# Kernel tuning notes

Measured on AMD Instinct MI355X. Metric: run time of the kernel, lower is better.

## Reference

```python
import jax, jax.numpy as jnp
import numpy as np

N0 = 1373      # hardcoded node-type split in the original forward
TAO = 0.4
EPS = 1e-12


def _l2norm(x, axis):
    # matches torch F.normalize(p=2): x / max(||x||, eps)
    n = jnp.sqrt(jnp.sum(x * x, axis=axis, keepdims=True))
    return x / jnp.maximum(n, EPS)


def setup_inputs() -> dict:
    key = jax.random.key(0)
    ks = jax.random.split(key, 12)
    N, E, D_IN, F, H, D = 20000, 320000, 256, 32, 8, 32
    feat = jax.random.normal(ks[0], (N, D_IN), jnp.float32)
    sloc = jax.random.normal(ks[1], (N, D), jnp.float32)
    topo_fea = jax.random.normal(ks[2], (N, D), jnp.float32)
    src = jax.random.randint(ks[3], (E,), 0, N)
    dst = jax.random.randint(ks[4], (E,), 0, N)
    e_feat = jax.random.randint(ks[5], (E,), 0, 4)
    s = 1.0 / np.sqrt(D_IN)
    W_proj0 = jax.random.normal(ks[6], (D_IN, H * F), jnp.float32) * s
    W_proj1 = jax.random.normal(ks[7], (D_IN, H * F), jnp.float32) * s
    W_prob = jax.random.normal(ks[8], (H, F, F), jnp.float32) * (1.0 / np.sqrt(F))
    W_res0 = jax.random.normal(ks[9], (D_IN, H * F), jnp.float32) * s
    W_res1 = jax.random.normal(ks[10], (D_IN, H * F), jnp.float32) * s
    etype_attn = jnp.ones((4,), jnp.float32)
    return dict(feat=feat, sloc=sloc, topo_fea=topo_fea, src=src, dst=dst,
                e_feat=e_feat, W_proj0=W_proj0, W_proj1=W_proj1, W_prob=W_prob,
                W_res0=W_res0, W_res1=W_res1, etype_attn=etype_attn)


def reference(feat, sloc, topo_fea, src, dst, e_feat,
              W_proj0, W_proj1, W_prob, W_res0, W_res1, etype_attn):
    N = feat.shape[0]
    H, F = W_prob.shape[0], W_prob.shape[2]
    sloc3 = sloc[:, None, :]        # (N,1,D) -- .unsqueeze(1)
    topo3 = topo_fea[:, None, :]

    # per-type node projection
    feat_src = jnp.concatenate(
        [feat[:N0] @ W_proj0, feat[N0:] @ W_proj1], axis=0).reshape(N, H, F)
    # per-head attention feature: softmax(tanh(fc4prob_i(.)), dim=feat)
    ft_attn = jax.nn.softmax(
        jnp.tanh(jnp.einsum('nhf,hfg->nhg', feat_src, W_prob)), axis=2)
    # F.normalize over the NODE dimension (dim=0), as in original
    ft_norm = _l2norm(feat_src, axis=0)

    sloc_n = _l2norm(sloc3, axis=2)
    topo_n = _l2norm(topo3, axis=2)

    # edge attention scores
    a = jnp.sum(ft_attn[dst] * ft_norm[src], axis=2, keepdims=True)   # (E,H,1)
    cos_s = jnp.sum(sloc_n[src] * sloc_n[dst], axis=2, keepdims=True)  # (E,1,1)
    cos_t = jnp.sum(topo_n[src] * topo_n[dst], axis=2, keepdims=True)
    sim = (TAO * cos_s + (1.0 - TAO) * cos_t + 1.0) / 2.0             # (E,1,1)
    e = (sim * a * etype_attn[e_feat][:, None, None])[:, :, 0]        # (E,H)

    # edge softmax: segment softmax over incoming edges of each dst node
    m = jax.ops.segment_max(e, dst, num_segments=N)                   # (N,H)
    ex = jnp.exp(e - m[dst])
    z = jax.ops.segment_sum(ex, dst, num_segments=N)
    att = ex / z[dst]                                                 # (E,H)

    # three u_mul_e + sum aggregations
    aw = att[:, :, None]                                              # (E,H,1)
    rst = jax.ops.segment_sum(feat_src[src] * aw, dst, num_segments=N)  # (N,H,F)
    sl2 = jax.ops.segment_sum(sloc3[src] * aw, dst, num_segments=N)     # (N,H,D)
    tp2 = jax.ops.segment_sum(topo3[src] * aw, dst, num_segments=N)     # (N,H,D)

    resval = jnp.concatenate(
        [feat[:N0] @ W_res0, feat[N0:] @ W_res1], axis=0).reshape(N, H, F)
    out_fea = jax.nn.relu(rst + resval).mean(axis=1)   # (N,F)
    out_sloc = (sl2 + sloc3).mean(axis=1)              # (N,D)
    out_topo = (tp2 + topo3).mean(axis=1)              # (N,D)
    return out_fea, out_sloc, out_topo
```

## Files before the change

kernel.cpp:

```cpp
#include <hip/hip_runtime.h>
#include <math.h>

#define HN0 1373
#define BM 128
#define BN 128
#define BK 32
#define LDT 40

typedef __attribute__((ext_vector_type(8))) short short8;
typedef __attribute__((ext_vector_type(4))) float f32x4;

__device__ inline unsigned short f2bf(float f) {
  unsigned int u = __float_as_uint(f);
  unsigned int r = (u + 0x7FFFu + ((u >> 16) & 1u)) >> 16;
  return (unsigned short)r;
}
__device__ inline float bflo(unsigned int u) { return __uint_as_float(u << 16); }
__device__ inline float bfhi(unsigned int u) { return __uint_as_float(u & 0xFFFF0000u); }

__device__ inline uint4 pack8bf(float4 a, float4 b) {
  uint4 o;
  o.x = (unsigned)f2bf(a.x) | ((unsigned)f2bf(a.y) << 16);
  o.y = (unsigned)f2bf(a.z) | ((unsigned)f2bf(a.w) << 16);
  o.z = (unsigned)f2bf(b.x) | ((unsigned)f2bf(b.y) << 16);
  o.w = (unsigned)f2bf(b.z) | ((unsigned)f2bf(b.w) << 16);
  return o;
}

__global__ __launch_bounds__(256) void prep(
    const float* __restrict__ Wp0, const float* __restrict__ Wr0,
    const float* __restrict__ Wp1, const float* __restrict__ Wr1,
    unsigned short* __restrict__ BTw,
    const float* __restrict__ sloc, const float* __restrict__ topo,
    float* __restrict__ inv_s, float* __restrict__ inv_t,
    unsigned short* __restrict__ slt,
    const int* __restrict__ dst, int* __restrict__ deg, int N, int E) {
  int b = blockIdx.x;
  int tid = threadIdx.x;
  int nodeBlocks = (N + 7) / 8;
  if (b < 1024) {
    int n = b & 511, g = b >> 9;
    const float* W;
    if (g == 0) W = (n < 256) ? Wp0 : Wr0;
    else        W = (n < 256) ? Wp1 : Wr1;
    int c = n & 255;
    BTw[(size_t)g * 512 * 256 + (size_t)n * 256 + tid] = f2bf(W[(size_t)tid * 256 + c]);
  } else if (b < 1024 + nodeBlocks) {
    int node = (b - 1024) * 8 + (tid >> 5);
    int d = tid & 31;
    if (node >= N) return;
    float s = sloc[(size_t)node * 32 + d];
    float t = topo[(size_t)node * 32 + d];
    float ss = s * s, tt = t * t;
#pragma unroll
    for (int m = 16; m >= 1; m >>= 1) {
      ss += __shfl_xor(ss, m);
      tt += __shfl_xor(tt, m);
    }
    if (d == 0) {
      inv_s[node] = 1.f / fmaxf(sqrtf(ss), 1e-12f);
      inv_t[node] = 1.f / fmaxf(sqrtf(tt), 1e-12f);
    }
    slt[(size_t)node * 64 + d] = f2bf(s);
    slt[(size_t)node * 64 + 32 + d] = f2bf(t);
  } else {
    int e = (b - 1024 - nodeBlocks) * 256 + tid;
    if (e < E) atomicAdd(&deg[dst[e]], 1);
  }
}

__global__ __launch_bounds__(256) void gemm_mfma(
    const float* __restrict__ A, const unsigned short* __restrict__ BTw,
    unsigned short* __restrict__ feat_bf, float* __restrict__ resval, int N) {
  __shared__ __align__(16) unsigned short As[BM * LDT];
  __shared__ __align__(16) unsigned short Bs[BN * LDT];
  int tid = threadIdx.x;
  int lane = tid & 63;
  int w = tid >> 6;
  int wr = w >> 1, wc = w & 1;

  int g0t = (HN0 + BM - 1) / BM;
  int bx = blockIdx.x;
  bool g1 = bx >= g0t;
  int rowBase = g1 ? HN0 + (bx - g0t) * BM : bx * BM;
  int rowEnd = g1 ? N : HN0;
  const unsigned short* BT = BTw + (g1 ? (size_t)512 * 256 : 0);
  int colBase = blockIdx.y * BN;

  int r0 = tid >> 2;
  int kp = (tid & 3) << 3;
  int ar1 = min(rowBase + r0, rowEnd - 1);
  int ar2 = min(rowBase + r0 + 64, rowEnd - 1);
  const float* aP1 = A + (size_t)ar1 * 256 + kp;
  const float* aP2 = A + (size_t)ar2 * 256 + kp;
  const unsigned short* bP1 = BT + (size_t)(colBase + r0) * 256 + kp;
  const unsigned short* bP2 = bP1 + (size_t)64 * 256;
  int wo1 = r0 * LDT + kp;
  int wo2 = (r0 + 64) * LDT + kp;

  int q = lane >> 4;
  int fr = lane & 15;
  int aOff = (wr * 64 + fr) * LDT + q * 8;
  int bOff = (wc * 64 + fr) * LDT + q * 8;

  f32x4 acc[4][4] = {};

  float4 fa1a = *reinterpret_cast<const float4*>(aP1);
  float4 fa1b = *reinterpret_cast<const float4*>(aP1 + 4);
  float4 fa2a = *reinterpret_cast<const float4*>(aP2);
  float4 fa2b = *reinterpret_cast<const float4*>(aP2 + 4);
  uint4 rb1 = *reinterpret_cast<const uint4*>(bP1);
  uint4 rb2 = *reinterpret_cast<const uint4*>(bP2);

  for (int t = 0; t < 8; ++t) {
    *reinterpret_cast<uint4*>(&As[wo1]) = pack8bf(fa1a, fa1b);
    *reinterpret_cast<uint4*>(&As[wo2]) = pack8bf(fa2a, fa2b);
    *reinterpret_cast<uint4*>(&Bs[wo1]) = rb1;
    *reinterpret_cast<uint4*>(&Bs[wo2]) = rb2;
    __syncthreads();
    if (t < 7) {
      int ko = (t + 1) * BK;
      fa1a = *reinterpret_cast<const float4*>(aP1 + ko);
      fa1b = *reinterpret_cast<const float4*>(aP1 + ko + 4);
      fa2a = *reinterpret_cast<const float4*>(aP2 + ko);
      fa2b = *reinterpret_cast<const float4*>(aP2 + ko + 4);
      rb1 = *reinterpret_cast<const uint4*>(bP1 + ko);
      rb2 = *reinterpret_cast<const uint4*>(bP2 + ko);
    }
    short8 af[4], bf4[4];
#pragma unroll
    for (int i = 0; i < 4; ++i) {
      af[i] = *reinterpret_cast<const short8*>(&As[aOff + i * 16 * LDT]);
      bf4[i] = *reinterpret_cast<const short8*>(&Bs[bOff + i * 16 * LDT]);
    }
#pragma unroll
    for (int i = 0; i < 4; ++i)
#pragma unroll
      for (int j = 0; j < 4; ++j)
        acc[i][j] = __builtin_amdgcn_mfma_f32_16x16x32_bf16(af[i], bf4[j], acc[i][j], 0, 0, 0);
    __syncthreads();
  }

  if (colBase < 256) {
#pragma unroll
    for (int i = 0; i < 4; ++i) {
      int rb = rowBase + wr * 64 + i * 16 + q * 4;
#pragma unroll
      for (int j = 0; j < 4; ++j) {
        int col = colBase + wc * 64 + j * 16 + fr;
        f32x4 v = acc[i][j];
#pragma unroll
        for (int rr = 0; rr < 4; ++rr) {
          int r = rb + rr;
          if (r < rowEnd) feat_bf[(size_t)r * 256 + col] = f2bf(v[rr]);
        }
      }
    }
  } else {
    int cOff = colBase - 256;
#pragma unroll
    for (int i = 0; i < 4; ++i) {
      int rb = rowBase + wr * 64 + i * 16 + q * 4;
#pragma unroll
      for (int j = 0; j < 4; ++j) {
        int col = cOff + wc * 64 + j * 16 + fr;
        f32x4 v = acc[i][j];
#pragma unroll
        for (int rr = 0; rr < 4; ++rr) {
          int r = rb + rr;
          if (r < rowEnd) resval[(size_t)r * 256 + col] = v[rr];
        }
      }
    }
  }
}

__global__ __launch_bounds__(256) void attn_probs(
    const unsigned short* __restrict__ feat_bf, const float* __restrict__ W_prob,
    unsigned short* __restrict__ ft_attn, float* __restrict__ col_ss, int N) {
  __shared__ float WL[8192];
  __shared__ float fsL[16 * 256];
  int tid = threadIdx.x;
  for (int i = tid; i < 8192; i += 256) WL[i] = W_prob[i];
  int nodeBase = blockIdx.x * 16;
  float ssp = 0.f;
  for (int i = 0; i < 16; ++i) {
    int n = nodeBase + i;
    float v = (n < N) ? __uint_as_float((unsigned)feat_bf[(size_t)n * 256 + tid] << 16) : 0.f;
    fsL[i * 256 + tid] = v;
    ssp += v * v;
  }
  atomicAdd(&col_ss[tid], ssp);
  __syncthreads();
  int h = tid >> 5, g = tid & 31;
  for (int i = 0; i < 16; ++i) {
    int n = nodeBase + i;
    if (n >= N) break;
    float t = 0.f;
    const float* wp = &WL[h * 1024 + g];
    const float* fr = &fsL[i * 256 + h * 32];
#pragma unroll
    for (int f = 0; f < 32; ++f) t = fmaf(fr[f], wp[f * 32], t);
    t = tanhf(t);
    float mx = t;
#pragma unroll
    for (int s = 16; s >= 1; s >>= 1) mx = fmaxf(mx, __shfl_xor(mx, s));
    float ex = __expf(t - mx);
    float sm = ex;
#pragma unroll
    for (int s = 16; s >= 1; s >>= 1) sm += __shfl_xor(sm, s);
    ft_attn[(size_t)n * 256 + tid] = f2bf(ex / sm);
  }
}

__global__ __launch_bounds__(512) void scan_block(const int* __restrict__ deg,
                                                  int* __restrict__ start,
                                                  int* __restrict__ bsum, int n) {
  __shared__ int buf[512];
  int tid = threadIdx.x;
  int gid = blockIdx.x * 512 + tid;
  int v = (gid < n) ? deg[gid] : 0;
  buf[tid] = v;
  __syncthreads();
  for (int off = 1; off < 512; off <<= 1) {
    int t = (tid >= off) ? buf[tid - off] : 0;
    __syncthreads();
    buf[tid] += t;
    __syncthreads();
  }
  if (gid < n) start[gid] = buf[tid] - v;
  if (tid == 511) bsum[blockIdx.x] = buf[511];
}

__global__ __launch_bounds__(256) void mid_small(float* __restrict__ col_ss,
                                                 int* __restrict__ bsum, int nb) {
  int tid = threadIdx.x;
  col_ss[tid] = 1.f / fmaxf(sqrtf(col_ss[tid]), 1e-12f);
  __shared__ int buf[128];
  if (tid < nb) buf[tid] = bsum[tid];
  __syncthreads();
  if (tid == 0) {
    int run = 0;
    for (int i = 0; i < nb; ++i) { int v = buf[i]; buf[i] = run; run += v; }
  }
  __syncthreads();
  if (tid < nb) bsum[tid] = buf[tid];
}

__global__ __launch_bounds__(256) void fill_sim(
    const int* __restrict__ src, const int* __restrict__ dst,
    const int* __restrict__ e_feat, const float* __restrict__ etype_attn,
    const unsigned short* __restrict__ slt,
    const float* __restrict__ inv_s, const float* __restrict__ inv_t,
    const int* __restrict__ start, const int* __restrict__ bsum,
    int* __restrict__ cursor, int* __restrict__ csr_src,
    float* __restrict__ csr_w, int E) {
  int tid = threadIdx.x;
  int j = tid & 7;
  int e = blockIdx.x * 32 + (tid >> 3);
  if (e >= E) return;
  int s = src[e], d = dst[e];
  const unsigned short* ps = slt + (size_t)s * 64 + j * 4;
  const unsigned short* pd = slt + (size_t)d * 64 + j * 4;
  uint2 sa = *reinterpret_cast<const uint2*>(ps);
  uint2 sb = *reinterpret_cast<const uint2*>(pd);
  uint2 ta = *reinterpret_cast<const uint2*>(ps + 32);
  uint2 tb = *reinterpret_cast<const uint2*>(pd + 32);
  float cs = bflo(sa.x) * bflo(sb.x) + bfhi(sa.x) * bfhi(sb.x) +
             bflo(sa.y) * bflo(sb.y) + bfhi(sa.y) * bfhi(sb.y);
  float ct = bflo(ta.x) * bflo(tb.x) + bfhi(ta.x) * bfhi(tb.x) +
             bflo(ta.y) * bflo(tb.y) + bfhi(ta.y) * bfhi(tb.y);
#pragma unroll
  for (int m = 4; m >= 1; m >>= 1) {
    cs += __shfl_xor(cs, m);
    ct += __shfl_xor(ct, m);
  }
  if (j == 0) {
    cs *= inv_s[s] * inv_s[d];
    ct *= inv_t[s] * inv_t[d];
    float sim = (0.4f * cs + 0.6f * ct + 1.f) * 0.5f;
    float wv = sim * etype_attn[e_feat[e]];
    int pos = start[d] + bsum[d >> 9] + atomicAdd(&cursor[d], 1);
    csr_src[pos] = s;
    csr_w[pos] = wv;
  }
}

#define GATHER(S, FP, SL, TP)                                                  \
  {                                                                            \
    FP = *reinterpret_cast<const uint2*>(feat_bf + (size_t)(S) * 256 + fb);    \
    const unsigned short* sp_ = slt + (size_t)(S) * 64 + db;                   \
    SL = *reinterpret_cast<const uint2*>(sp_);                                 \
    TP = *reinterpret_cast<const uint2*>(sp_ + 32);                            \
  }

#define CONSUME(FP, SL, TP, WV)                                                \
  {                                                                            \
    float fs0 = bflo(FP.x), fs1 = bfhi(FP.x);                                  \
    float fs2 = bflo(FP.y), fs3 = bfhi(FP.y);                                  \
    float pa = ai4.x * fs0 + ai4.y * fs1 + ai4.z * fs2 + ai4.w * fs3;          \
    pa += __shfl_xor(pa, 1);                                                   \
    pa += __shfl_xor(pa, 2);                                                   \
    pa += __shfl_xor(pa, 4);                                                   \
    float p = __expf(pa * WV);                                                 \
    l += p;                                                                    \
    accf.x = fmaf(p, fs0, accf.x); accf.y = fmaf(p, fs1, accf.y);              \
    accf.z = fmaf(p, fs2, accf.z); accf.w = fmaf(p, fs3, accf.w);              \
    accs.x = fmaf(p, bflo(SL.x), accs.x); accs.y = fmaf(p, bfhi(SL.x), accs.y);\
    accs.z = fmaf(p, bflo(SL.y), accs.z); accs.w = fmaf(p, bfhi(SL.y), accs.w);\
    acct.x = fmaf(p, bflo(TP.x), acct.x); acct.y = fmaf(p, bfhi(TP.x), acct.y);\
    acct.z = fmaf(p, bflo(TP.y), acct.z); acct.w = fmaf(p, bfhi(TP.y), acct.w);\
  }

__global__ __launch_bounds__(256) void edge_aggregate(
    const unsigned short* __restrict__ feat_bf, const float* __restrict__ resval,
    const unsigned short* __restrict__ ft_attn, const float* __restrict__ inv_cn,
    const unsigned short* __restrict__ slt,
    const float* __restrict__ sloc, const float* __restrict__ topo,
    const int* __restrict__ start, const int* __restrict__ bsum,
    const int* __restrict__ deg,
    const int* __restrict__ csr_src, const float* __restrict__ csr_w,
    float* __restrict__ out, int N) {
  int wave = threadIdx.x >> 6;
  int n = blockIdx.x * 4 + wave;
  if (n >= N) return;
  int lane = threadIdx.x & 63;
  int j = lane & 7;
  int fb = (lane >> 3) * 32 + j * 4;
  int db = j * 4;

  uint2 at2 = *reinterpret_cast<const uint2*>(ft_attn + (size_t)n * 256 + fb);
  float4 icn4 = *reinterpret_cast<const float4*>(inv_cn + fb);
  float4 ai4 = make_float4(bflo(at2.x) * icn4.x, bfhi(at2.x) * icn4.y,
                           bflo(at2.y) * icn4.z, bfhi(at2.y) * icn4.w);
  float l = 0.f;
  float4 accf = make_float4(0.f, 0.f, 0.f, 0.f);
  float4 accs = make_float4(0.f, 0.f, 0.f, 0.f);
  float4 acct = make_float4(0.f, 0.f, 0.f, 0.f);
  int s0 = start[n] + bsum[n >> 9];
  int dg = deg[n];

  int sA = 0, sB = 0;
  float wA = 0.f, wB = 0.f;
  uint2 fpA, slA, tpA, fpB, slB, tpB;
  fpA = fpB = slA = slB = tpA = tpB = make_uint2(0u, 0u);
  if (dg > 0) {
    sA = csr_src[s0]; wA = csr_w[s0];
    GATHER(sA, fpA, slA, tpA);
  }
  if (dg > 1) {
    sB = csr_src[s0 + 1]; wB = csr_w[s0 + 1];
    GATHER(sB, fpB, slB, tpB);
  }
  int i = 0;
  for (; i + 1 < dg; i += 2) {
    CONSUME(fpA, slA, tpA, wA);
    if (i + 2 < dg) {
      sA = csr_src[s0 + i + 2]; wA = csr_w[s0 + i + 2];
      GATHER(sA, fpA, slA, tpA);
    }
    CONSUME(fpB, slB, tpB, wB);
    if (i + 3 < dg) {
      sB = csr_src[s0 + i + 3]; wB = csr_w[s0 + i + 3];
      GATHER(sB, fpB, slB, tpB);
    }
  }
  if (i < dg) CONSUME(fpA, slA, tpA, wA);

  float invl = (l > 0.f) ? 1.f / l : 0.f;

  float4 res4 = *reinterpret_cast<const float4*>(resval + (size_t)n * 256 + fb);
  float4 of = make_float4(fmaxf(fmaf(accf.x, invl, res4.x), 0.f),
                          fmaxf(fmaf(accf.y, invl, res4.y), 0.f),
                          fmaxf(fmaf(accf.z, invl, res4.z), 0.f),
                          fmaxf(fmaf(accf.w, invl, res4.w), 0.f));
  float4 os = make_float4(accs.x * invl, accs.y * invl, accs.z * invl, accs.w * invl);
  float4 ot = make_float4(acct.x * invl, acct.y * invl, acct.z * invl, acct.w * invl);
#pragma unroll
  for (int msk = 8; msk <= 32; msk <<= 1) {
    of.x += __shfl_xor(of.x, msk); of.y += __shfl_xor(of.y, msk);
    of.z += __shfl_xor(of.z, msk); of.w += __shfl_xor(of.w, msk);
    os.x += __shfl_xor(os.x, msk); os.y += __shfl_xor(os.y, msk);
    os.z += __shfl_xor(os.z, msk); os.w += __shfl_xor(os.w, msk);
    ot.x += __shfl_xor(ot.x, msk); ot.y += __shfl_xor(ot.y, msk);
    ot.z += __shfl_xor(ot.z, msk); ot.w += __shfl_xor(ot.w, msk);
  }
  if (lane < 8) {
    float4 sln = *reinterpret_cast<const float4*>(sloc + (size_t)n * 32 + db);
    float4 tpn = *reinterpret_cast<const float4*>(topo + (size_t)n * 32 + db);
    float4 o0 = make_float4(of.x * 0.125f, of.y * 0.125f, of.z * 0.125f, of.w * 0.125f);
    float4 o1 = make_float4(fmaf(os.x, 0.125f, sln.x), fmaf(os.y, 0.125f, sln.y),
                            fmaf(os.z, 0.125f, sln.z), fmaf(os.w, 0.125f, sln.w));
    float4 o2 = make_float4(fmaf(ot.x, 0.125f, tpn.x), fmaf(ot.y, 0.125f, tpn.y),
                            fmaf(ot.z, 0.125f, tpn.z), fmaf(ot.w, 0.125f, tpn.w));
    *reinterpret_cast<float4*>(out + (size_t)n * 32 + db) = o0;
    *reinterpret_cast<float4*>(out + (size_t)N * 32 + (size_t)n * 32 + db) = o1;
    *reinterpret_cast<float4*>(out + (size_t)2 * N * 32 + (size_t)n * 32 + db) = o2;
  }
}

extern "C" void kernel_launch(void* const* d_in, const int* in_sizes, int n_in,
                              void* d_out, int out_size, void* d_ws, size_t ws_size,
                              hipStream_t stream) {
  const float* feat = (const float*)d_in[0];
  const float* sloc = (const float*)d_in[1];
  const float* topo = (const float*)d_in[2];
  const int* src = (const int*)d_in[3];
  const int* dst = (const int*)d_in[4];
  const int* e_feat = (const int*)d_in[5];
  const float* W_proj0 = (const float*)d_in[6];
  const float* W_proj1 = (const float*)d_in[7];
  const float* W_prob = (const float*)d_in[8];
  const float* W_res0 = (const float*)d_in[9];
  const float* W_res1 = (const float*)d_in[10];
  const float* etype_attn = (const float*)d_in[11];
  int E = in_sizes[3];
  int N = in_sizes[1] / 32;
  float* out = (float*)d_out;

  char* ws = (char*)d_ws;
  size_t off = 0;
  auto alloc = [&](size_t bytes) -> char* {
    char* p = ws + off;
    off += (bytes + 255) & ~(size_t)255;
    return p;
  };
  int* deg = (int*)alloc((size_t)N * 4);
  int* cursor = (int*)alloc((size_t)N * 4);
  float* col_ss = (float*)alloc(256 * 4);
  size_t zeroBytes = ((char*)col_ss + 256 * 4) - (char*)deg;
  int* startArr = (int*)alloc(((size_t)N + 1) * 4);
  int* bsum = (int*)alloc(128 * 4);
  float* inv_s = (float*)alloc((size_t)N * 4);
  float* inv_t = (float*)alloc((size_t)N * 4);
  int* csr_src = (int*)alloc((size_t)E * 4);
  float* csr_w = (float*)alloc((size_t)E * 4);
  unsigned short* feat_bf = (unsigned short*)alloc((size_t)N * 256 * 2);
  unsigned short* slt = (unsigned short*)alloc((size_t)N * 64 * 2);
  float* resval = (float*)alloc((size_t)N * 256 * 4);
  unsigned short* ft_attn = (unsigned short*)alloc((size_t)N * 256 * 2);
  unsigned short* BTw = (unsigned short*)alloc((size_t)2 * 512 * 256 * 2);

  hipMemsetAsync(deg, 0, zeroBytes, stream);

  int nodeBlocks = (N + 7) / 8;
  int degBlocks = (E + 255) / 256;
  prep<<<1024 + nodeBlocks + degBlocks, 256, 0, stream>>>(
      W_proj0, W_res0, W_proj1, W_res1, BTw, sloc, topo, inv_s, inv_t, slt,
      dst, deg, N, E);

  int g0t = (HN0 + BM - 1) / BM;
  int g1t = (N - HN0 + BM - 1) / BM;
  gemm_mfma<<<dim3(g0t + g1t, 4), 256, 0, stream>>>(feat, BTw, feat_bf, resval, N);

  attn_probs<<<(N + 15) / 16, 256, 0, stream>>>(feat_bf, W_prob, ft_attn, col_ss, N);

  int nb = (N + 511) / 512;
  scan_block<<<nb, 512, 0, stream>>>(deg, startArr, bsum, N);
  mid_small<<<1, 256, 0, stream>>>(col_ss, bsum, nb);

  fill_sim<<<(E + 31) / 32, 256, 0, stream>>>(src, dst, e_feat, etype_attn, slt,
                                              inv_s, inv_t, startArr, bsum,
                                              cursor, csr_src, csr_w, E);

  edge_aggregate<<<(N + 3) / 4, 256, 0, stream>>>(feat_bf, resval, ft_attn, col_ss,
                                                  slt, sloc, topo, startArr, bsum, deg,
                                                  csr_src, csr_w, out, N);
}
```

Before: 191.0 us.

## Fuse cosine-similarity edge weight into aggregation and split each node across two waves

The per-edge cosine similarity is no longer computed in the CSR fill kernel. The edge aggregation kernel now computes it from the already-gathered source sloc/topo rows against the destination row kept in registers. The CSR stores a packed src index plus edge type in one int, inverse norms are packed as two bf16 values, and the slt layout is interleaved so one 16-byte load gets both sloc and topo. Each destination node is also split across two waves that handle alternating edges and combine partial sums through shared memory. This removes a gather-heavy pass and its float weight array, at the cost of a block-wide barrier, bf16-rounded norms, and a 28-bit limit on the source index.

```diff
diff --git a/kernel.cpp b/kernel.cpp
--- a/kernel.cpp
+++ b/kernel.cpp
@@ -32,7 +32,7 @@
     const float* __restrict__ Wp1, const float* __restrict__ Wr1,
     unsigned short* __restrict__ BTw,
     const float* __restrict__ sloc, const float* __restrict__ topo,
-    float* __restrict__ inv_s, float* __restrict__ inv_t,
+    unsigned int* __restrict__ invp,
     unsigned short* __restrict__ slt,
     const int* __restrict__ dst, int* __restrict__ deg, int N, int E) {
   int b = blockIdx.x;
@@ -58,11 +58,13 @@
       tt += __shfl_xor(tt, m);
     }
     if (d == 0) {
-      inv_s[node] = 1.f / fmaxf(sqrtf(ss), 1e-12f);
-      inv_t[node] = 1.f / fmaxf(sqrtf(tt), 1e-12f);
-    }
-    slt[(size_t)node * 64 + d] = f2bf(s);
-    slt[(size_t)node * 64 + 32 + d] = f2bf(t);
+      float is = 1.f / fmaxf(sqrtf(ss), 1e-12f);
+      float it = 1.f / fmaxf(sqrtf(tt), 1e-12f);
+      invp[node] = (unsigned)f2bf(is) | ((unsigned)f2bf(it) << 16);
+    }
+    int base = (size_t)0 + (d >> 2) * 8 + (d & 3);
+    slt[(size_t)node * 64 + base] = f2bf(s);
+    slt[(size_t)node * 64 + base + 4] = f2bf(t);
   } else {
     int e = (b - 1024 - nodeBlocks) * 256 + tid;
     if (e < E) atomicAdd(&deg[dst[e]], 1);
@@ -247,125 +249,138 @@
   if (tid < nb) bsum[tid] = buf[tid];
 }
 
-__global__ __launch_bounds__(256) void fill_sim(
+__global__ __launch_bounds__(256) void fill_csr(
     const int* __restrict__ src, const int* __restrict__ dst,
-    const int* __restrict__ e_feat, const float* __restrict__ etype_attn,
-    const unsigned short* __restrict__ slt,
-    const float* __restrict__ inv_s, const float* __restrict__ inv_t,
+    const int* __restrict__ e_feat,
     const int* __restrict__ start, const int* __restrict__ bsum,
-    int* __restrict__ cursor, int* __restrict__ csr_src,
-    float* __restrict__ csr_w, int E) {
-  int tid = threadIdx.x;
-  int j = tid & 7;
-  int e = blockIdx.x * 32 + (tid >> 3);
+    int* __restrict__ cursor, int* __restrict__ csr, int E) {
+  int e = blockIdx.x * 256 + threadIdx.x;
   if (e >= E) return;
-  int s = src[e], d = dst[e];
-  const unsigned short* ps = slt + (size_t)s * 64 + j * 4;
-  const unsigned short* pd = slt + (size_t)d * 64 + j * 4;
-  uint2 sa = *reinterpret_cast<const uint2*>(ps);
-  uint2 sb = *reinterpret_cast<const uint2*>(pd);
-  uint2 ta = *reinterpret_cast<const uint2*>(ps + 32);
-  uint2 tb = *reinterpret_cast<const uint2*>(pd + 32);
-  float cs = bflo(sa.x) * bflo(sb.x) + bfhi(sa.x) * bfhi(sb.x) +
-             bflo(sa.y) * bflo(sb.y) + bfhi(sa.y) * bfhi(sb.y);
-  float ct = bflo(ta.x) * bflo(tb.x) + bfhi(ta.x) * bfhi(tb.x) +
-             bflo(ta.y) * bflo(tb.y) + bfhi(ta.y) * bfhi(tb.y);
-#pragma unroll
-  for (int m = 4; m >= 1; m >>= 1) {
-    cs += __shfl_xor(cs, m);
-    ct += __shfl_xor(ct, m);
-  }
-  if (j == 0) {
-    cs *= inv_s[s] * inv_s[d];
-    ct *= inv_t[s] * inv_t[d];
-    float sim = (0.4f * cs + 0.6f * ct + 1.f) * 0.5f;
-    float wv = sim * etype_attn[e_feat[e]];
-    int pos = start[d] + bsum[d >> 9] + atomicAdd(&cursor[d], 1);
-    csr_src[pos] = s;
-    csr_w[pos] = wv;
-  }
-}
-
-#define GATHER(S, FP, SL, TP)                                                  \
-  {                                                                            \
-    FP = *reinterpret_cast<const uint2*>(feat_bf + (size_t)(S) * 256 + fb);    \
-    const unsigned short* sp_ = slt + (size_t)(S) * 64 + db;                   \
-    SL = *reinterpret_cast<const uint2*>(sp_);                                 \
-    TP = *reinterpret_cast<const uint2*>(sp_ + 32);                            \
-  }
-
-#define CONSUME(FP, SL, TP, WV)                                                \
-  {                                                                            \
+  int d = dst[e];
+  int pos = start[d] + bsum[d >> 9] + atomicAdd(&cursor[d], 1);
+  csr[pos] = src[e] | (e_feat[e] << 28);
+}
+
+#define LOADIDX(K, V, W, IV)                                                   \
+  do {                                                                         \
+    V = csr[s0 + half + 2 * (K)];                                              \
+    int k_ = ((unsigned)V) >> 28;                                              \
+    W = (k_ & 1) ? ((k_ & 2) ? et3 : et1) : ((k_ & 2) ? et2 : et0);            \
+    IV = invp[V & 0x0FFFFFFF];                                                 \
+  } while (0)
+
+#define GATHER(V, FP, Q)                                                       \
+  do {                                                                         \
+    int s_ = (V) & 0x0FFFFFFF;                                                 \
+    FP = *reinterpret_cast<const uint2*>(feat_bf + (size_t)s_ * 256 + fb);     \
+    Q = *reinterpret_cast<const uint4*>(slt + (size_t)s_ * 64 + j * 8);        \
+  } while (0)
+
+#define CONSUME(W, IV, FP, Q)                                                  \
+  do {                                                                         \
     float fs0 = bflo(FP.x), fs1 = bfhi(FP.x);                                  \
     float fs2 = bflo(FP.y), fs3 = bfhi(FP.y);                                  \
+    float sl0 = bflo(Q.x), sl1 = bfhi(Q.x), sl2 = bflo(Q.y), sl3 = bfhi(Q.y);  \
+    float tp0 = bflo(Q.z), tp1 = bfhi(Q.z), tp2 = bflo(Q.w), tp3 = bfhi(Q.w);  \
     float pa = ai4.x * fs0 + ai4.y * fs1 + ai4.z * fs2 + ai4.w * fs3;          \
-    pa += __shfl_xor(pa, 1);                                                   \
-    pa += __shfl_xor(pa, 2);                                                   \
-    pa += __shfl_xor(pa, 4);                                                   \
-    float p = __expf(pa * WV);                                                 \
+    float cs = sl0 * sld.x + sl1 * sld.y + sl2 * sld.z + sl3 * sld.w;          \
+    float ct = tp0 * tpd.x + tp1 * tpd.y + tp2 * tpd.z + tp3 * tpd.w;          \
+    float u = c_s0 * bflo(IV) * cs + c_t0 * bfhi(IV) * ct;                     \
+    pa += __shfl_xor(pa, 1); u += __shfl_xor(u, 1);                            \
+    pa += __shfl_xor(pa, 2); u += __shfl_xor(u, 2);                            \
+    pa += __shfl_xor(pa, 4); u += __shfl_xor(u, 4);                            \
+    float sim = fmaf(u, 0.5f, 0.5f);                                           \
+    float p = __expf(pa * sim * (W));                                          \
     l += p;                                                                    \
     accf.x = fmaf(p, fs0, accf.x); accf.y = fmaf(p, fs1, accf.y);              \
     accf.z = fmaf(p, fs2, accf.z); accf.w = fmaf(p, fs3, accf.w);              \
-    accs.x = fmaf(p, bflo(SL.x), accs.x); accs.y = fmaf(p, bfhi(SL.x), accs.y);\
-    accs.z = fmaf(p, bflo(SL.y), accs.z); accs.w = fmaf(p, bfhi(SL.y), accs.w);\
-    acct.x = fmaf(p, bflo(TP.x), acct.x); acct.y = fmaf(p, bfhi(TP.x), acct.y);\
-    acct.z = fmaf(p, bflo(TP.y), acct.z); acct.w = fmaf(p, bfhi(TP.y), acct.w);\
-  }
+    accs.x = fmaf(p, sl0, accs.x); accs.y = fmaf(p, sl1, accs.y);              \
+    accs.z = fmaf(p, sl2, accs.z); accs.w = fmaf(p, sl3, accs.w);              \
+    acct.x = fmaf(p, tp0, acct.x); acct.y = fmaf(p, tp1, acct.y);              \
+    acct.z = fmaf(p, tp2, acct.z); acct.w = fmaf(p, tp3, acct.w);              \
+  } while (0)
 
 __global__ __launch_bounds__(256) void edge_aggregate(
     const unsigned short* __restrict__ feat_bf, const float* __restrict__ resval,
     const unsigned short* __restrict__ ft_attn, const float* __restrict__ inv_cn,
-    const unsigned short* __restrict__ slt,
+    const unsigned short* __restrict__ slt, const unsigned int* __restrict__ invp,
     const float* __restrict__ sloc, const float* __restrict__ topo,
+    const float* __restrict__ etype_attn,
     const int* __restrict__ start, const int* __restrict__ bsum,
-    const int* __restrict__ deg,
-    const int* __restrict__ csr_src, const float* __restrict__ csr_w,
+    const int* __restrict__ deg, const int* __restrict__ csr,
     float* __restrict__ out, int N) {
-  int wave = threadIdx.x >> 6;
-  int n = blockIdx.x * 4 + wave;
-  if (n >= N) return;
+  __shared__ float comb[2][13][64];
+  int wv = threadIdx.x >> 6;
+  int pr = wv >> 1;
+  int half = wv & 1;
+  int n = blockIdx.x * 2 + pr;
+  bool valid = n < N;
   int lane = threadIdx.x & 63;
   int j = lane & 7;
   int fb = (lane >> 3) * 32 + j * 4;
   int db = j * 4;
 
-  uint2 at2 = *reinterpret_cast<const uint2*>(ft_attn + (size_t)n * 256 + fb);
-  float4 icn4 = *reinterpret_cast<const float4*>(inv_cn + fb);
-  float4 ai4 = make_float4(bflo(at2.x) * icn4.x, bfhi(at2.x) * icn4.y,
-                           bflo(at2.y) * icn4.z, bfhi(at2.y) * icn4.w);
   float l = 0.f;
   float4 accf = make_float4(0.f, 0.f, 0.f, 0.f);
   float4 accs = make_float4(0.f, 0.f, 0.f, 0.f);
   float4 acct = make_float4(0.f, 0.f, 0.f, 0.f);
-  int s0 = start[n] + bsum[n >> 9];
-  int dg = deg[n];
-
-  int sA = 0, sB = 0;
-  float wA = 0.f, wB = 0.f;
-  uint2 fpA, slA, tpA, fpB, slB, tpB;
-  fpA = fpB = slA = slB = tpA = tpB = make_uint2(0u, 0u);
-  if (dg > 0) {
-    sA = csr_src[s0]; wA = csr_w[s0];
-    GATHER(sA, fpA, slA, tpA);
-  }
-  if (dg > 1) {
-    sB = csr_src[s0 + 1]; wB = csr_w[s0 + 1];
-    GATHER(sB, fpB, slB, tpB);
-  }
-  int i = 0;
-  for (; i + 1 < dg; i += 2) {
-    CONSUME(fpA, slA, tpA, wA);
-    if (i + 2 < dg) {
-      sA = csr_src[s0 + i + 2]; wA = csr_w[s0 + i + 2];
-      GATHER(sA, fpA, slA, tpA);
-    }
-    CONSUME(fpB, slB, tpB, wB);
-    if (i + 3 < dg) {
-      sB = csr_src[s0 + i + 3]; wB = csr_w[s0 + i + 3];
-      GATHER(sB, fpB, slB, tpB);
-    }
-  }
-  if (i < dg) CONSUME(fpA, slA, tpA, wA);
+  float4 ai4 = make_float4(0.f, 0.f, 0.f, 0.f);
+  float4 sld = make_float4(0.f, 0.f, 0.f, 0.f);
+  float4 tpd = make_float4(0.f, 0.f, 0.f, 0.f);
+
+  float et0 = etype_attn[0], et1 = etype_attn[1];
+  float et2 = etype_attn[2], et3 = etype_attn[3];
+
+  if (valid) {
+    uint2 at2 = *reinterpret_cast<const uint2*>(ft_attn + (size_t)n * 256 + fb);
+    float4 icn4 = *reinterpret_cast<const float4*>(inv_cn + fb);
+    ai4 = make_float4(bflo(at2.x) * icn4.x, bfhi(at2.x) * icn4.y,
+                      bflo(at2.y) * icn4.z, bfhi(at2.y) * icn4.w);
+    sld = *reinterpret_cast<const float4*>(sloc + (size_t)n * 32 + db);
+    tpd = *reinterpret_cast<const float4*>(topo + (size_t)n * 32 + db);
+    unsigned int ivd = invp[n];
+    float c_s0 = 0.4f * bflo(ivd);
+    float c_t0 = 0.6f * bfhi(ivd);
+    int s0 = start[n] + bsum[n >> 9];
+    int dg = deg[n];
+    int cnt = (dg > half) ? ((dg - half + 1) >> 1) : 0;
+
+    int vA = 0, vB = 0;
+    float wA = 0.f, wB = 0.f;
+    unsigned int ivA = 0u, ivB = 0u;
+    uint2 fpA = make_uint2(0u, 0u), fpB = make_uint2(0u, 0u);
+    uint4 qA = make_uint4(0u, 0u, 0u, 0u), qB = make_uint4(0u, 0u, 0u, 0u);
+    if (cnt > 0) { LOADIDX(0, vA, wA, ivA); GATHER(vA, fpA, qA); }
+    if (cnt > 1) { LOADIDX(1, vB, wB, ivB); GATHER(vB, fpB, qB); }
+    int k = 0;
+    for (; k + 1 < cnt; k += 2) {
+      CONSUME(wA, ivA, fpA, qA);
+      if (k + 2 < cnt) { LOADIDX(k + 2, vA, wA, ivA); GATHER(vA, fpA, qA); }
+      CONSUME(wB, ivB, fpB, qB);
+      if (k + 3 < cnt) { LOADIDX(k + 3, vB, wB, ivB); GATHER(vB, fpB, qB); }
+    }
+    if (k < cnt) CONSUME(wA, ivA, fpA, qA);
+  }
+
+  if (half == 1) {
+    comb[pr][0][lane] = l;
+    comb[pr][1][lane] = accf.x; comb[pr][2][lane] = accf.y;
+    comb[pr][3][lane] = accf.z; comb[pr][4][lane] = accf.w;
+    comb[pr][5][lane] = accs.x; comb[pr][6][lane] = accs.y;
+    comb[pr][7][lane] = accs.z; comb[pr][8][lane] = accs.w;
+    comb[pr][9][lane] = acct.x; comb[pr][10][lane] = acct.y;
+    comb[pr][11][lane] = acct.z; comb[pr][12][lane] = acct.w;
+  }
+  __syncthreads();
+  if (half == 1 || !valid) return;
+
+  l += comb[pr][0][lane];
+  accf.x += comb[pr][1][lane]; accf.y += comb[pr][2][lane];
+  accf.z += comb[pr][3][lane]; accf.w += comb[pr][4][lane];
+  accs.x += comb[pr][5][lane]; accs.y += comb[pr][6][lane];
+  accs.z += comb[pr][7][lane]; accs.w += comb[pr][8][lane];
+  acct.x += comb[pr][9][lane]; acct.y += comb[pr][10][lane];
+  acct.z += comb[pr][11][lane]; acct.w += comb[pr][12][lane];
 
   float invl = (l > 0.f) ? 1.f / l : 0.f;
 
@@ -386,13 +401,11 @@
     ot.z += __shfl_xor(ot.z, msk); ot.w += __shfl_xor(ot.w, msk);
   }
   if (lane < 8) {
-    float4 sln = *reinterpret_cast<const float4*>(sloc + (size_t)n * 32 + db);
-    float4 tpn = *reinterpret_cast<const float4*>(topo + (size_t)n * 32 + db);
     float4 o0 = make_float4(of.x * 0.125f, of.y * 0.125f, of.z * 0.125f, of.w * 0.125f);
-    float4 o1 = make_float4(fmaf(os.x, 0.125f, sln.x), fmaf(os.y, 0.125f, sln.y),
-                            fmaf(os.z, 0.125f, sln.z), fmaf(os.w, 0.125f, sln.w));
-    float4 o2 = make_float4(fmaf(ot.x, 0.125f, tpn.x), fmaf(ot.y, 0.125f, tpn.y),
-                            fmaf(ot.z, 0.125f, tpn.z), fmaf(ot.w, 0.125f, tpn.w));
+    float4 o1 = make_float4(fmaf(os.x, 0.125f, sld.x), fmaf(os.y, 0.125f, sld.y),
+                            fmaf(os.z, 0.125f, sld.z), fmaf(os.w, 0.125f, sld.w));
+    float4 o2 = make_float4(fmaf(ot.x, 0.125f, tpd.x), fmaf(ot.y, 0.125f, tpd.y),
+                            fmaf(ot.z, 0.125f, tpd.z), fmaf(ot.w, 0.125f, tpd.w));
     *reinterpret_cast<float4*>(out + (size_t)n * 32 + db) = o0;
     *reinterpret_cast<float4*>(out + (size_t)N * 32 + (size_t)n * 32 + db) = o1;
     *reinterpret_cast<float4*>(out + (size_t)2 * N * 32 + (size_t)n * 32 + db) = o2;
@@ -431,10 +444,8 @@
   size_t zeroBytes = ((char*)col_ss + 256 * 4) - (char*)deg;
   int* startArr = (int*)alloc(((size_t)N + 1) * 4);
   int* bsum = (int*)alloc(128 * 4);
-  float* inv_s = (float*)alloc((size_t)N * 4);
-  float* inv_t = (float*)alloc((size_t)N * 4);
-  int* csr_src = (int*)alloc((size_t)E * 4);
-  float* csr_w = (float*)alloc((size_t)E * 4);
+  unsigned int* invp = (unsigned int*)alloc((size_t)N * 4);
+  int* csr = (int*)alloc((size_t)E * 4);
   unsigned short* feat_bf = (unsigned short*)alloc((size_t)N * 256 * 2);
   unsigned short* slt = (unsigned short*)alloc((size_t)N * 64 * 2);
   float* resval = (float*)alloc((size_t)N * 256 * 4);
@@ -446,7 +457,7 @@
   int nodeBlocks = (N + 7) / 8;
   int degBlocks = (E + 255) / 256;
   prep<<<1024 + nodeBlocks + degBlocks, 256, 0, stream>>>(
-      W_proj0, W_res0, W_proj1, W_res1, BTw, sloc, topo, inv_s, inv_t, slt,
+      W_proj0, W_res0, W_proj1, W_res1, BTw, sloc, topo, invp, slt,
       dst, deg, N, E);
 
   int g0t = (HN0 + BM - 1) / BM;
@@ -459,11 +470,10 @@
   scan_block<<<nb, 512, 0, stream>>>(deg, startArr, bsum, N);
   mid_small<<<1, 256, 0, stream>>>(col_ss, bsum, nb);
 
-  fill_sim<<<(E + 31) / 32, 256, 0, stream>>>(src, dst, e_feat, etype_attn, slt,
-                                              inv_s, inv_t, startArr, bsum,
-                                              cursor, csr_src, csr_w, E);
-
-  edge_aggregate<<<(N + 3) / 4, 256, 0, stream>>>(feat_bf, resval, ft_attn, col_ss,
-                                                  slt, sloc, topo, startArr, bsum, deg,
-                                                  csr_src, csr_w, out, N);
-}
+  fill_csr<<<(E + 255) / 256, 256, 0, stream>>>(src, dst, e_feat, startArr, bsum,
+                                                cursor, csr, E);
+
+  edge_aggregate<<<(N + 1) / 2, 256, 0, stream>>>(feat_bf, resval, ft_attn, col_ss,
+                                                  slt, invp, sloc, topo, etype_attn,
+                                                  startArr, bsum, deg, csr, out, N);
+}
```

Result: slower. 214.9 us (+12.5%).
